# Performance work log

Measured on AMD Instinct MI355X. Metric: run time of the kernel, lower is better.

The kernel has to match this reference:

```python
import jax, jax.numpy as jnp
import numpy as np

SRC_V, TRG_V = 36616, 23262
EMB, ENC_H, DEC_H = 300, 512, 1024
S, T, B = 50, 50, 128


def setup_inputs() -> dict:
    key = jax.random.key(0)
    ks = jax.random.split(key, 17)
    sc = 0.05
    n = lambda k, shp: (jax.random.normal(k, shp, jnp.float32) * sc)
    return {
        "input_src_batch": jax.random.randint(ks[0], (S, B), 0, SRC_V),
        "input_trg_batch": jax.random.randint(ks[1], (T, B), 0, TRG_V),
        "EEMB": n(ks[2], (SRC_V, EMB)),
        "enc_Wih_f": n(ks[3], (4 * ENC_H, EMB)),
        "enc_Whh_f": n(ks[4], (4 * ENC_H, ENC_H)),
        "enc_b_f": n(ks[5], (4 * ENC_H,)),
        "enc_Wih_r": n(ks[6], (4 * ENC_H, EMB)),
        "enc_Whh_r": n(ks[7], (4 * ENC_H, ENC_H)),
        "enc_b_r": n(ks[8], (4 * ENC_H,)),
        "attn_Wi": n(ks[9], (DEC_H, DEC_H)),
        "attn_Wo": n(ks[10], (DEC_H, 2 * DEC_H)),
        "dec_Wih": n(ks[11], (4 * DEC_H, DEC_H + EMB)),
        "dec_Whh": n(ks[12], (4 * DEC_H, DEC_H)),
        "dec_b": n(ks[13], (4 * DEC_H,)),
        "DEMB": n(ks[14], (TRG_V, EMB)),
        "gen_W": n(ks[15], (TRG_V, DEC_H)),
        "gen_b": n(ks[16], (TRG_V,)),
    }


def lstm_step(h, c, x, Wih, Whh, b):
    # PyTorch gate order: i, f, g, o
    g = x @ Wih.T + h @ Whh.T + b
    i, f, gg, o = jnp.split(g, 4, axis=-1)
    c2 = jax.nn.sigmoid(f) * c + jax.nn.sigmoid(i) * jnp.tanh(gg)
    h2 = jax.nn.sigmoid(o) * jnp.tanh(c2)
    return h2, c2


def reference(input_src_batch, input_trg_batch, EEMB, enc_Wih_f, enc_Whh_f,
              enc_b_f, enc_Wih_r, enc_Whh_r, enc_b_r, attn_Wi, attn_Wo,
              dec_Wih, dec_Whh, dec_b, DEMB, gen_W, gen_b):
    batch = input_src_batch.shape[1]
    sent_len = input_trg_batch.shape[0]
    emb = EEMB[input_src_batch]  # [S, B, 300]

    def scan_dir(xs, Wih, Whh, b):
        def f(carry, x):
            h, c = carry
            h2, c2 = lstm_step(h, c, x, Wih, Whh, b)
            return (h2, c2), h2
        init = (jnp.zeros((batch, ENC_H), emb.dtype),
                jnp.zeros((batch, ENC_H), emb.dtype))
        (hF, cF), hs = jax.lax.scan(f, init, xs)
        return hs, hF, cF

    hs_f, hF, cF = scan_dir(emb, enc_Wih_f, enc_Whh_f, enc_b_f)
    hs_r, hR, cR = scan_dir(emb[::-1], enc_Wih_r, enc_Whh_r, enc_b_r)
    hs_r = hs_r[::-1]
    enc_out = jnp.concatenate([hs_f, hs_r], axis=-1)  # [S, B, 1024]
    # torch permute(1,2,0).view(B,1024) interleaves fwd/rev per feature
    hidden = jnp.stack([hF, hR], axis=-1).reshape(batch, DEC_H)
    context = jnp.stack([cF, cR], axis=-1).reshape(batch, DEC_H)

    def attn(h):
        semi = h @ attn_Wi.T                                # [B,1024]
        score = jnp.einsum('sbd,bd->sb', enc_out, semi)     # [S,B]
        alpha = jax.nn.softmax(score, axis=0)               # softmax over src len
        s_tilde = jnp.einsum('sb,sbd->bd', alpha, enc_out)  # [B,1024]
        return jnp.tanh(jnp.concatenate([s_tilde, h], axis=1) @ attn_Wo.T)

    trg_emb = DEMB[input_trg_batch[: sent_len - 1]]  # [T-1, B, 300]

    def step(carry, x_emb):
        h, c = carry
        c_t = attn(h)
        dec_in = jnp.concatenate([c_t, x_emb], axis=1)  # [B, 1324]
        h2, c2 = lstm_step(h, c, dec_in, dec_Wih, dec_Whh, dec_b)
        logp = jax.nn.log_softmax(h2 @ gen_W.T + gen_b, axis=1)
        return (h2, c2), logp

    _, outs = jax.lax.scan(step, (hidden, context), trg_emb)  # [T-1,B,V]
    out0 = jnp.zeros((1, batch, TRG_V), outs.dtype)
    return jnp.concatenate([out0, outs], axis=0)  # [T, B, V]
```

## Files before the change

kernel.cpp:

```cpp
#include <hip/hip_runtime.h>
#include <hip/hip_bf16.h>

#define S_LEN 50
#define T_LEN 50
#define BATCH 128
#define EMB 300
#define ENC_H 512
#define DEC_H 1024
#define TRG_V 23262
#define DEC_IN (DEC_H + EMB)
#define KCAT (DEC_IN + DEC_H)
#define GN (4 * DEC_H)

static inline int cdiv(int a, int b) { return (a + b - 1) / b; }

__device__ __forceinline__ float sigm(float x) { return 1.f / (1.f + expf(-x)); }

typedef __attribute__((ext_vector_type(8))) short bf16x8;
typedef __attribute__((ext_vector_type(4))) float f32x4;

__device__ __forceinline__ void gload_lds16(const void* g, void* l) {
    __builtin_amdgcn_global_load_lds((const __attribute__((address_space(1))) int*)g,
                                     (__attribute__((address_space(3))) int*)l, 16, 0, 0);
}

__device__ __forceinline__ float cload1(const float* p) {
    return __hip_atomic_load(p, __ATOMIC_RELAXED, __HIP_MEMORY_SCOPE_AGENT);
}
__device__ __forceinline__ float2 cload2(const float* p) {
    unsigned long long u = __hip_atomic_load((const unsigned long long*)p,
                                             __ATOMIC_RELAXED, __HIP_MEMORY_SCOPE_AGENT);
    union U { unsigned long long u; float2 f; } c; c.u = u; return c.f;
}
__device__ __forceinline__ float4 cload4(const float* p) {
    float2 a = cload2(p), b = cload2(p + 2);
    return make_float4(a.x, a.y, b.x, b.y);
}
__device__ __forceinline__ void cstore1(float* p, float v) {
    __hip_atomic_store(p, v, __ATOMIC_RELAXED, __HIP_MEMORY_SCOPE_AGENT);
}
__device__ __forceinline__ void cstore2(float* p, float2 v) {
    union U { unsigned long long u; float2 f; } c; c.f = v;
    __hip_atomic_store((unsigned long long*)p, c.u, __ATOMIC_RELAXED, __HIP_MEMORY_SCOPE_AGENT);
}
__device__ __forceinline__ void cstore4(float* p, float4 v) {
    cstore2(p, make_float2(v.x, v.y)); cstore2(p + 2, make_float2(v.z, v.w));
}

__device__ __forceinline__ void gbar(unsigned* cnt, unsigned target) {
    __syncthreads();
    if (threadIdx.x == 0) {
        atomicAdd(cnt, 1u);
        while (atomicAdd(cnt, 0u) < target)
            __builtin_amdgcn_s_sleep(32);
    }
    __syncthreads();
}

__global__ __launch_bounds__(256)
void gemm_mfma_bf16(const __hip_bfloat16* __restrict__ A, const __hip_bfloat16* __restrict__ W,
                    const float* __restrict__ bias, float* __restrict__ C,
                    int M, int N, int K, int ldc)
{
    __shared__ short As[128 * 32];
    __shared__ short Bs[128 * 32];
    const int tid  = threadIdx.x;
    const int wave = tid >> 6;
    const int lane = tid & 63;
    const int m0 = blockIdx.y * 128;
    const int n0 = blockIdx.x * 128;
    const int wr = wave >> 1, wc = wave & 1;

    const int srow = lane >> 2;
    const int kgrp = lane & 3;
    const int arow0 = 32 * wave;

    f32x4 acc[4][4] = {};

    for (int k0 = 0; k0 < K; k0 += 32) {
#pragma unroll
        for (int c = 0; c < 2; c++) {
            int row = arow0 + 16 * c + srow;
            gload_lds16(A + (size_t)(m0 + row) * K + k0 + kgrp * 8,
                        &As[(arow0 + 16 * c) * 32]);
        }
#pragma unroll
        for (int c = 0; c < 2; c++) {
            int row = arow0 + 16 * c + srow;
            int gr = n0 + row; if (gr > N - 1) gr = N - 1;
            gload_lds16(W + (size_t)gr * K + k0 + kgrp * 8,
                        &Bs[(arow0 + 16 * c) * 32]);
        }
        __syncthreads();

        bf16x8 a[4], b[4];
#pragma unroll
        for (int mi = 0; mi < 4; mi++)
            a[mi] = *(const bf16x8*)&As[(wr * 64 + mi * 16 + (lane & 15)) * 32 + (lane >> 4) * 8];
#pragma unroll
        for (int ni = 0; ni < 4; ni++)
            b[ni] = *(const bf16x8*)&Bs[(wc * 64 + ni * 16 + (lane & 15)) * 32 + (lane >> 4) * 8];
#pragma unroll
        for (int mi = 0; mi < 4; mi++)
#pragma unroll
            for (int ni = 0; ni < 4; ni++)
                acc[mi][ni] = __builtin_amdgcn_mfma_f32_16x16x32_bf16(a[mi], b[ni], acc[mi][ni], 0, 0, 0);
        __syncthreads();
    }

#pragma unroll
    for (int mi = 0; mi < 4; mi++)
#pragma unroll
        for (int ni = 0; ni < 4; ni++) {
            int col = n0 + wc * 64 + ni * 16 + (lane & 15);
            if (col >= N) continue;
            float bv = bias[col];
#pragma unroll
            for (int r = 0; r < 4; r++) {
                int row = m0 + wr * 64 + mi * 16 + (lane >> 4) * 4 + r;
                C[(size_t)row * ldc + col] = acc[mi][ni][r] + bv;
            }
        }
}

__global__ void cast_f32_bf16(const float* __restrict__ in, __hip_bfloat16* __restrict__ out, size_t n)
{
    size_t i = ((size_t)blockIdx.x * blockDim.x + threadIdx.x) * 4;
    if (i + 3 < n) {
        float4 v = *(const float4*)(in + i);
        out[i + 0] = __float2bfloat16(v.x);
        out[i + 1] = __float2bfloat16(v.y);
        out[i + 2] = __float2bfloat16(v.z);
        out[i + 3] = __float2bfloat16(v.w);
    } else {
        for (; i < n; i++) out[i] = __float2bfloat16(in[i]);
    }
}

template<int BM, int BN, int BK, int TM, int TN, bool HAS_BIAS>
__global__ __launch_bounds__((BM / TM) * (BN / TN))
void gemm_bt(const float* __restrict__ A, const float* __restrict__ W,
             const float* __restrict__ bias, float* __restrict__ C,
             int M, int N, int K, int ldc)
{
    constexpr int NT  = (BM / TM) * (BN / TN);
    constexpr int NGA = TM / 4;
    constexpr int NGB = TN / 4;
    constexpr int GS  = (BN / TN) * 4;
    constexpr int LPA = BM * BK / 4 / NT;
    constexpr int LPB = BN * BK / 4 / NT;

    __shared__ float As[BK][BM + 4];
    __shared__ float Bs[BK][BN + 4];

    const int tid = threadIdx.x;
    const int tx = tid % (BN / TN);
    const int ty = tid / (BN / TN);
    const int m0 = blockIdx.y * BM;
    const int n0 = blockIdx.x * BN;

    float acc[TM][TN];
#pragma unroll
    for (int i = 0; i < TM; i++)
#pragma unroll
        for (int j = 0; j < TN; j++) acc[i][j] = 0.f;

    for (int k0 = 0; k0 < K; k0 += BK) {
#pragma unroll
        for (int e = 0; e < LPA; e++) {
            int idx = tid + e * NT;
            int r = idx / (BK / 4);
            int c4 = idx % (BK / 4);
            int row = m0 + r; if (row > M - 1) row = M - 1;
            int kk = k0 + c4 * 4;
            float4 v;
            if (kk + 3 < K) {
                v = *(const float4*)(A + (size_t)row * K + kk);
            } else {
                v.x = (kk + 0 < K) ? A[(size_t)row * K + kk + 0] : 0.f;
                v.y = (kk + 1 < K) ? A[(size_t)row * K + kk + 1] : 0.f;
                v.z = (kk + 2 < K) ? A[(size_t)row * K + kk + 2] : 0.f;
                v.w = (kk + 3 < K) ? A[(size_t)row * K + kk + 3] : 0.f;
            }
            As[c4 * 4 + 0][r] = v.x; As[c4 * 4 + 1][r] = v.y;
            As[c4 * 4 + 2][r] = v.z; As[c4 * 4 + 3][r] = v.w;
        }
#pragma unroll
        for (int e = 0; e < LPB; e++) {
            int idx = tid + e * NT;
            int r = idx / (BK / 4);
            int c4 = idx % (BK / 4);
            int row = n0 + r; if (row > N - 1) row = N - 1;
            int kk = k0 + c4 * 4;
            float4 v;
            if (kk + 3 < K) {
                v = *(const float4*)(W + (size_t)row * K + kk);
            } else {
                v.x = (kk + 0 < K) ? W[(size_t)row * K + kk + 0] : 0.f;
                v.y = (kk + 1 < K) ? W[(size_t)row * K + kk + 1] : 0.f;
                v.z = (kk + 2 < K) ? W[(size_t)row * K + kk + 2] : 0.f;
                v.w = (kk + 3 < K) ? W[(size_t)row * K + kk + 3] : 0.f;
            }
            Bs[c4 * 4 + 0][r] = v.x; Bs[c4 * 4 + 1][r] = v.y;
            Bs[c4 * 4 + 2][r] = v.z; Bs[c4 * 4 + 3][r] = v.w;
        }
        __syncthreads();
#pragma unroll
        for (int kk = 0; kk < BK; kk++) {
            float a[TM], b[TN];
#pragma unroll
            for (int g = 0; g < NGA; g++) {
                float4 v = *(const float4*)(&As[kk][ty * TM + g * 4]);
                a[g * 4 + 0] = v.x; a[g * 4 + 1] = v.y; a[g * 4 + 2] = v.z; a[g * 4 + 3] = v.w;
            }
#pragma unroll
            for (int g = 0; g < NGB; g++) {
                float4 v = *(const float4*)(&Bs[kk][tx * 4 + g * GS]);
                b[g * 4 + 0] = v.x; b[g * 4 + 1] = v.y; b[g * 4 + 2] = v.z; b[g * 4 + 3] = v.w;
            }
#pragma unroll
            for (int i = 0; i < TM; i++)
#pragma unroll
                for (int j = 0; j < TN; j++)
                    acc[i][j] = fmaf(a[i], b[j], acc[i][j]);
        }
        __syncthreads();
    }

#pragma unroll
    for (int i = 0; i < TM; i++) {
        int row = m0 + ty * TM + i;
        if (row >= M) continue;
#pragma unroll
        for (int g = 0; g < NGB; g++) {
            int colb = n0 + tx * 4 + g * GS;
#pragma unroll
            for (int j = 0; j < 4; j++) {
                int cc = colb + j;
                if (cc >= N) continue;
                float v = acc[i][g * 4 + j];
                if (HAS_BIAS) v += bias[cc];
                C[(size_t)row * ldc + cc] = v;
            }
        }
    }
}

__device__ __forceinline__ float4 g4k(const float* base, int kk, int K) {
    float4 v = make_float4(0.f, 0.f, 0.f, 0.f);
    if (kk + 3 < K) v = *(const float4*)(base + kk);
    else {
        if (kk     < K) v.x = base[kk];
        if (kk + 1 < K) v.y = base[kk + 1];
        if (kk + 2 < K) v.z = base[kk + 2];
    }
    return v;
}
__device__ __forceinline__ float4 g4kc(const float* base, int kk, int K) {
    float4 v = make_float4(0.f, 0.f, 0.f, 0.f);
    if (kk + 3 < K) v = cload4(base + kk);
    else {
        if (kk     < K) v.x = cload1(base + kk);
        if (kk + 1 < K) v.y = cload1(base + kk + 1);
        if (kk + 2 < K) v.z = cload1(base + kk + 2);
    }
    return v;
}

__device__ __forceinline__ void tile_core(
    float (&As)[2][32][36], float (&Bs)[2][32][68],
    const float* __restrict__ A, int lda,
    const float* __restrict__ W, int ldw, int K,
    int m0, int n0, float (&acc)[2][4])
{
    const int tid = threadIdx.x;
    const int tx = tid & 15, ty = tid >> 4;
    const int ar = tid >> 3, ac4 = tid & 7;
    const float* abase = A + (size_t)(m0 + ar) * lda;
    const float* bb0   = W + (size_t)(n0 + ar) * ldw;
    const float* bb1   = bb0 + (size_t)32 * ldw;

    acc[0][0]=acc[0][1]=acc[0][2]=acc[0][3]=0.f;
    acc[1][0]=acc[1][1]=acc[1][2]=acc[1][3]=0.f;
    const int NIT = (K + 31) / 32;

    float4 pa0, pb00, pb10;
    float4 pa1, pb01, pb11;

    auto LOAD = [&](int itx, float4& qa, float4& qb0, float4& qb1) {
        int k0 = itx * 32, kk = k0 + ac4 * 4;
        if (k0 + 32 <= K) {
            qa = cload4(abase + kk); qb0 = *(const float4*)(bb0 + kk); qb1 = *(const float4*)(bb1 + kk);
        } else {
            qa = g4kc(abase, kk, K); qb0 = g4k(bb0, kk, K); qb1 = g4k(bb1, kk, K);
        }
    };
    auto SLDS = [&](int nb, const float4& qa, const float4& qb0, const float4& qb1) {
        *(float4*)&As[nb][ar][ac4 * 4] = qa;
        Bs[nb][ac4*4+0][ar]    = qb0.x; Bs[nb][ac4*4+1][ar]    = qb0.y;
        Bs[nb][ac4*4+2][ar]    = qb0.z; Bs[nb][ac4*4+3][ar]    = qb0.w;
        Bs[nb][ac4*4+0][ar+32] = qb1.x; Bs[nb][ac4*4+1][ar+32] = qb1.y;
        Bs[nb][ac4*4+2][ar+32] = qb1.z; Bs[nb][ac4*4+3][ar+32] = qb1.w;
    };
    auto COMP = [&](int c) {
#pragma unroll
        for (int k4 = 0; k4 < 8; ++k4) {
            float4 a0 = *(const float4*)&As[c][ty*2+0][k4*4];
            float4 a1 = *(const float4*)&As[c][ty*2+1][k4*4];
            float4 b0 = *(const float4*)&Bs[c][k4*4+0][tx*4];
            float4 b1 = *(const float4*)&Bs[c][k4*4+1][tx*4];
            float4 b2 = *(const float4*)&Bs[c][k4*4+2][tx*4];
            float4 b3 = *(const float4*)&Bs[c][k4*4+3][tx*4];
            float av0[4] = {a0.x, a0.y, a0.z, a0.w};
            float av1[4] = {a1.x, a1.y, a1.z, a1.w};
            float4 bq[4] = {b0, b1, b2, b3};
#pragma unroll
            for (int q = 0; q < 4; q++) {
                acc[0][0] = fmaf(av0[q], bq[q].x, acc[0][0]);
                acc[0][1] = fmaf(av0[q], bq[q].y, acc[0][1]);
                acc[0][2] = fmaf(av0[q], bq[q].z, acc[0][2]);
                acc[0][3] = fmaf(av0[q], bq[q].w, acc[0][3]);
                acc[1][0] = fmaf(av1[q], bq[q].x, acc[1][0]);
                acc[1][1] = fmaf(av1[q], bq[q].y, acc[1][1]);
                acc[1][2] = fmaf(av1[q], bq[q].z, acc[1][2]);
                acc[1][3] = fmaf(av1[q], bq[q].w, acc[1][3]);
            }
        }
    };

    LOAD(0, pa0, pb00, pb10);
    if (NIT > 1) LOAD(1, pa1, pb01, pb11);
    SLDS(0, pa0, pb00, pb10);
    __syncthreads();

    int cur = 0;
    int it = 0;
    while (it < NIT) {
        if (it + 2 < NIT) LOAD(it + 2, pa0, pb00, pb10);
        COMP(cur);
        if (it + 1 < NIT) SLDS(cur ^ 1, pa1, pb01, pb11);
        __syncthreads();
        cur ^= 1; ++it;
        if (it >= NIT) break;
        if (it + 2 < NIT) LOAD(it + 2, pa1, pb01, pb11);
        COMP(cur);
        if (it + 1 < NIT) SLDS(cur ^ 1, pa0, pb00, pb10);
        __syncthreads();
        cur ^= 1; ++it;
    }
}

__device__ __forceinline__ void attn_body(
    int b, float* hv, float* sc,
    const float* __restrict__ encP, const float* __restrict__ enc_out,
    float* __restrict__ attn_cat)
{
    const int tid = threadIdx.x;
    for (int d = tid; d < DEC_H; d += 256) hv[d] = cload1(&attn_cat[(size_t)b * 2 * DEC_H + DEC_H + d]);
    __syncthreads();
    int wave = tid >> 6, lane = tid & 63;
    for (int s = wave; s < S_LEN; s += 4) {
        const float* e = encP + ((size_t)s * BATCH + b) * DEC_H;
        float p = 0.f;
        for (int d = lane; d < DEC_H; d += 64) p = fmaf(e[d], hv[d], p);
        for (int off = 32; off; off >>= 1) p += __shfl_down(p, off);
        if (lane == 0) sc[s] = p;
    }
    __syncthreads();
    if (tid < 64) {
        float x = (tid < S_LEN) ? sc[tid] : -1e30f;
        float m = x;
        for (int off = 32; off; off >>= 1) m = fmaxf(m, __shfl_xor(m, off));
        float ex = (tid < S_LEN) ? expf(x - m) : 0.f;
        float ssum = ex;
        for (int off = 32; off; off >>= 1) ssum += __shfl_xor(ssum, off);
        if (tid < S_LEN) sc[tid] = ex / ssum;
    }
    __syncthreads();
    for (int d = tid; d < DEC_H; d += 256) {
        float a = 0.f;
#pragma unroll 5
        for (int s = 0; s < S_LEN; s++)
            a = fmaf(sc[s], enc_out[((size_t)s * BATCH + b) * DEC_H + d], a);
        cstore1(&attn_cat[(size_t)b * 2 * DEC_H + d], a);
    }
}

__global__ __launch_bounds__(256)
void enc_persistent(const float* __restrict__ Gf, const float* __restrict__ Gr,
                    const float* __restrict__ whhF, const float* __restrict__ whhR,
                    float* __restrict__ hF2, float* __restrict__ hR2,
                    float* __restrict__ cF, float* __restrict__ cR,
                    float* __restrict__ enc_out, unsigned* __restrict__ barcnt)
{
    __shared__ struct { float As[2][32][36]; float Bs[2][32][68]; } sm;
    const int blk = blockIdx.x;
    const int tid = threadIdx.x;
    const int tx = tid & 15, ty = tid >> 4;
    const int dir = blk >> 7;
    const int id  = blk & 127;
    const int m0 = (id >> 5) * 32;
    const int n0 = (id & 31) * 64;
    const float* W  = dir ? whhR : whhF;
    float* cst      = dir ? cR : cF;
    float* hbase    = dir ? hR2 : hF2;
    const float* G  = dir ? Gr : Gf;
    const int HS = BATCH * ENC_H;
    unsigned epoch = 0;
    float acc[2][4];

    for (int t = 0; t < S_LEN; ++t) {
        const float* h_in = hbase + (size_t)(t & 1) * HS;
        float* h_out      = hbase + (size_t)((t + 1) & 1) * HS;
        int s_g = dir ? (S_LEN - 1 - t) : t;
        const float* D = G + (size_t)s_g * BATCH * 4 * ENC_H;

        tile_core(sm.As, sm.Bs, h_in, ENC_H, W, ENC_H, ENC_H, m0, n0, acc);

        int cb = n0 + tx * 4, j = cb >> 2;
#pragma unroll
        for (int i = 0; i < 2; i++) {
            int b = m0 + ty * 2 + i;
            float4 d4 = *(const float4*)(D + (size_t)b * 4 * ENC_H + cb);
            float gi = acc[i][0] + d4.x, gf = acc[i][1] + d4.y;
            float gg = acc[i][2] + d4.z, go = acc[i][3] + d4.w;
            float c2 = sigm(gf) * cst[b * ENC_H + j] + sigm(gi) * tanhf(gg);
            float h2 = sigm(go) * tanhf(c2);
            cst[b * ENC_H + j] = c2;
            cstore1(&h_out[b * ENC_H + j], h2);
            enc_out[((size_t)s_g * BATCH + b) * DEC_H + dir * ENC_H + j] = h2;
        }
        if (t < S_LEN - 1) gbar(barcnt, 256u * (++epoch));
    }
}

__global__ __launch_bounds__(256)
void dec_persistent(const float* __restrict__ encP, const float* __restrict__ enc_out,
                    const int* __restrict__ trg, const float* __restrict__ DEMB,
                    const float* __restrict__ aWo, const float* __restrict__ wcat,
                    const float* __restrict__ db_i,
                    float* __restrict__ attn_cat, float* __restrict__ catA,
                    float* __restrict__ cdec, float* __restrict__ gpart,
                    __hip_bfloat16* __restrict__ H_bf, unsigned* __restrict__ barcnt)
{
    __shared__ union {
        struct { float hv[DEC_H]; float sc[S_LEN]; } a;
        struct { float As[2][32][36]; float Bs[2][32][68]; } g;
    } sm;
    const int blk = blockIdx.x;
    const int tid = threadIdx.x;
    const int tx = tid & 15, ty = tid >> 4;
    unsigned epoch = 0;
    float acc[2][4];

    for (int t = 0; t < T_LEN - 1; ++t) {
        if (blk < 128) {
            attn_body(blk, sm.a.hv, sm.a.sc, encP, enc_out, attn_cat);
        } else if (blk < 192) {
            int id = blk - 128;
            int m0 = (id >> 4) * 32, n0 = (id & 15) * 64;
            tile_core(sm.g.As, sm.g.Bs, attn_cat + DEC_H, 2 * DEC_H,
                      aWo + DEC_H, 2 * DEC_H, DEC_H, m0, n0, acc);
            int cb = n0 + tx * 4;
#pragma unroll
            for (int i = 0; i < 2; i++) {
                int row = m0 + ty * 2 + i;
                cstore4(catA + (size_t)row * KCAT + cb,
                        make_float4(acc[i][0], acc[i][1], acc[i][2], acc[i][3]));
            }
        } else {
            int tau = blk - 192;
            int m0 = (tau >> 6) * 32, n0 = (tau & 63) * 64;
            tile_core(sm.g.As, sm.g.Bs, catA + DEC_H, KCAT,
                      wcat + DEC_H, KCAT, KCAT - DEC_H, m0, n0, acc);
            int cb = n0 + tx * 4;
#pragma unroll
            for (int i = 0; i < 2; i++) {
                int row = m0 + ty * 2 + i;
                cstore4(gpart + (size_t)row * GN + cb,
                        make_float4(acc[i][0], acc[i][1], acc[i][2], acc[i][3]));
            }
        }
        gbar(barcnt, 256u * (++epoch));

        if (blk < 64) {
            int m0 = (blk >> 4) * 32, n0 = (blk & 15) * 64;
            tile_core(sm.g.As, sm.g.Bs, attn_cat, 2 * DEC_H, aWo, 2 * DEC_H, DEC_H, m0, n0, acc);
            int cb = n0 + tx * 4;
#pragma unroll
            for (int i = 0; i < 2; i++) {
                int row = m0 + ty * 2 + i;
                float* dst = catA + (size_t)row * KCAT + cb;
                float4 prev = cload4(dst);
                cstore4(dst, make_float4(tanhf(acc[i][0] + prev.x), tanhf(acc[i][1] + prev.y),
                                         tanhf(acc[i][2] + prev.z), tanhf(acc[i][3] + prev.w)));
            }
        } else {
            int tau = blk;
            int m0 = (tau >> 6) * 32, n0 = (tau & 63) * 64;
            tile_core(sm.g.As, sm.g.Bs, catA + DEC_H, KCAT,
                      wcat + DEC_H, KCAT, KCAT - DEC_H, m0, n0, acc);
            int cb = n0 + tx * 4;
#pragma unroll
            for (int i = 0; i < 2; i++) {
                int row = m0 + ty * 2 + i;
                cstore4(gpart + (size_t)row * GN + cb,
                        make_float4(acc[i][0], acc[i][1], acc[i][2], acc[i][3]));
            }
        }
        gbar(barcnt, 256u * (++epoch));

        {
            int m0 = (blk >> 6) * 32, n0 = (blk & 63) * 64;
            tile_core(sm.g.As, sm.g.Bs, catA, KCAT, wcat, KCAT, DEC_H, m0, n0, acc);
            int cb = n0 + tx * 4, j = cb >> 2;
            float4 bz = *(const float4*)(db_i + cb);
#pragma unroll
            for (int i = 0; i < 2; i++) {
                int b = m0 + ty * 2 + i;
                float4 gp = cload4(gpart + (size_t)b * GN + cb);
                float gi = acc[i][0] + gp.x + bz.x, gf = acc[i][1] + gp.y + bz.y;
                float gg = acc[i][2] + gp.z + bz.z, go = acc[i][3] + gp.w + bz.w;
                float c2 = sigm(gf) * cdec[b * DEC_H + j] + sigm(gi) * tanhf(gg);
                float h2 = sigm(go) * tanhf(c2);
                cdec[b * DEC_H + j] = c2;
                H_bf[(size_t)t * BATCH * DEC_H + b * DEC_H + j] = __float2bfloat16(h2);
                cstore1(&attn_cat[(size_t)b * 2 * DEC_H + DEC_H + j], h2);
                cstore1(&catA[(size_t)b * KCAT + DEC_IN + j], h2);
            }
            if ((blk & 63) == 0 && t + 1 < T_LEN - 1) {
                for (int idx = tid; idx < 32 * EMB; idx += 256) {
                    int r = m0 + idx / EMB, e = idx % EMB;
                    int idt = trg[(t + 1) * BATCH + r];
                    cstore1(&catA[(size_t)r * KCAT + DEC_H + e], DEMB[(size_t)idt * EMB + e]);
                }
            }
        }
        if (t < T_LEN - 2) gbar(barcnt, 256u * (++epoch));
    }
}

__global__ void zero_f32(float* p, size_t n) {
    size_t i = (size_t)blockIdx.x * blockDim.x + threadIdx.x;
    if (i < n) p[i] = 0.f;
}

__global__ void gather_rows(const int* __restrict__ ids, const float* __restrict__ E,
                            float* __restrict__ out, int nrows, int width)
{
    size_t i = (size_t)blockIdx.x * blockDim.x + threadIdx.x;
    size_t total = (size_t)nrows * width;
    if (i >= total) return;
    int r = (int)(i / width);
    int e = (int)(i % width);
    out[i] = E[(size_t)ids[r] * width + e];
}

__global__ void interleave_rows(const float* __restrict__ src, float* __restrict__ dst,
                                int units, int kdim)
{
    size_t i = (size_t)blockIdx.x * blockDim.x + threadIdx.x;
    size_t total = (size_t)4 * units * kdim;
    if (i >= total) return;
    int ir = (int)(i / kdim), k = (int)(i % kdim);
    int gate = ir & 3, j = ir >> 2;
    dst[i] = src[(size_t)(gate * units + j) * kdim + k];
}

__global__ void interleave_vec(const float* __restrict__ src, float* __restrict__ dst, int units)
{
    int i = blockIdx.x * blockDim.x + threadIdx.x;
    if (i >= 4 * units) return;
    int gate = i & 3, j = i >> 2;
    dst[i] = src[gate * units + j];
}

__global__ void build_wcat_int(const float* __restrict__ Wih, const float* __restrict__ Whh,
                               float* __restrict__ dst)
{
    size_t i = (size_t)blockIdx.x * blockDim.x + threadIdx.x;
    if (i >= (size_t)4 * DEC_H * KCAT) return;
    int ir = (int)(i / KCAT), k = (int)(i % KCAT);
    int gate = ir & 3, j = ir >> 2;
    int r = gate * DEC_H + j;
    dst[i] = (k < DEC_IN) ? Wih[(size_t)r * DEC_IN + k] : Whh[(size_t)r * DEC_H + (k - DEC_IN)];
}

__global__ void transpose_sq(const float* __restrict__ src, float* __restrict__ dst, int n)
{
    int i = blockIdx.x * blockDim.x + threadIdx.x;
    if (i >= n * n) return;
    int r = i / n, c = i % n;
    dst[(size_t)r * n + c] = src[(size_t)c * n + r];
}

__global__ void dec_init2(const float* __restrict__ hF, const float* __restrict__ cF,
                          const float* __restrict__ hR, const float* __restrict__ cR,
                          const int* __restrict__ trg, const float* __restrict__ DEMB,
                          float* __restrict__ attn_cat, float* __restrict__ catA,
                          float* __restrict__ cdec)
{
    int idx = blockIdx.x * blockDim.x + threadIdx.x;
    if (idx < BATCH * DEC_H) {
        int b = idx / DEC_H, j = idx % DEC_H;
        int half = j >> 1;
        float h = (j & 1) ? hR[b * ENC_H + half] : hF[b * ENC_H + half];
        float c = (j & 1) ? cR[b * ENC_H + half] : cF[b * ENC_H + half];
        attn_cat[(size_t)b * 2 * DEC_H + DEC_H + j] = h;
        catA[(size_t)b * KCAT + DEC_IN + j] = h;
        cdec[idx] = c;
    } else {
        int i = idx - BATCH * DEC_H;
        if (i >= BATCH * EMB) return;
        int b = i / EMB, e = i % EMB;
        catA[(size_t)b * KCAT + DEC_H + e] = DEMB[(size_t)trg[b] * EMB + e];
    }
}

__global__ __launch_bounds__(256)
void log_softmax_rows(float* __restrict__ X, int V)
{
    int row = blockIdx.x;
    float* x = X + (size_t)row * V;
    int tid = threadIdx.x;
    __shared__ float redm[4], reds[4];
    float m = -1e30f;
    for (int i = tid; i < V; i += 256) m = fmaxf(m, x[i]);
    for (int off = 32; off; off >>= 1) m = fmaxf(m, __shfl_xor(m, off));
    if ((tid & 63) == 0) redm[tid >> 6] = m;
    __syncthreads();
    m = fmaxf(fmaxf(redm[0], redm[1]), fmaxf(redm[2], redm[3]));
    float s = 0.f;
    for (int i = tid; i < V; i += 256) s += expf(x[i] - m);
    for (int off = 32; off; off >>= 1) s += __shfl_xor(s, off);
    if ((tid & 63) == 0) reds[tid >> 6] = s;
    __syncthreads();
    s = reds[0] + reds[1] + reds[2] + reds[3];
    float lg = m + logf(s);
    for (int i = tid; i < V; i += 256) x[i] -= lg;
}

static void launch_gemm_big_bias(const float* A, const float* W, const float* bias, float* C,
                                 int M, int N, int K, int ldc, hipStream_t s)
{
    dim3 g(cdiv(N, 128), cdiv(M, 128), 1);
    gemm_bt<128, 128, 16, 8, 8, true><<<g, 256, 0, s>>>(A, W, bias, C, M, N, K, ldc);
}
static void launch_gemm_big(const float* A, const float* W, float* C,
                            int M, int N, int K, int ldc, hipStream_t s)
{
    dim3 g(cdiv(N, 128), cdiv(M, 128), 1);
    gemm_bt<128, 128, 16, 8, 8, false><<<g, 256, 0, s>>>(A, W, nullptr, C, M, N, K, ldc);
}

extern "C" void kernel_launch(void* const* d_in, const int* in_sizes, int n_in,
                              void* d_out, int out_size, void* d_ws, size_t ws_size,
                              hipStream_t stream)
{
    const int*   src   = (const int*)d_in[0];
    const int*   trg   = (const int*)d_in[1];
    const float* EEMBp = (const float*)d_in[2];
    const float* eWihF = (const float*)d_in[3];
    const float* eWhhF = (const float*)d_in[4];
    const float* ebF   = (const float*)d_in[5];
    const float* eWihR = (const float*)d_in[6];
    const float* eWhhR = (const float*)d_in[7];
    const float* ebR   = (const float*)d_in[8];
    const float* aWi   = (const float*)d_in[9];
    const float* aWo   = (const float*)d_in[10];
    const float* dWih  = (const float*)d_in[11];
    const float* dWhh  = (const float*)d_in[12];
    const float* db    = (const float*)d_in[13];
    const float* DEMBp = (const float*)d_in[14];
    const float* gW    = (const float*)d_in[15];
    const float* gb    = (const float*)d_in[16];
    float* out = (float*)d_out;
    float* ws  = (float*)d_ws;

    size_t off = 0;
    auto alloc = [&](size_t n) { float* p = ws + off; off += n; return p; };

    float* Gf      = alloc((size_t)S_LEN * BATCH * 4 * ENC_H);
    float* Gr      = alloc((size_t)S_LEN * BATCH * 4 * ENC_H);
    float* emb_src = alloc((size_t)S_LEN * BATCH * EMB);
    float* enc_out = alloc((size_t)S_LEN * BATCH * DEC_H);
    float* hF2     = alloc((size_t)2 * BATCH * ENC_H);
    float* hR2     = alloc((size_t)2 * BATCH * ENC_H);
    float* cF      = alloc(BATCH * ENC_H);
    float* cR      = alloc(BATCH * ENC_H);
    float* wihF_i  = alloc((size_t)4 * ENC_H * EMB);
    float* wihR_i  = alloc((size_t)4 * ENC_H * EMB);
    float* whhF_i  = alloc((size_t)4 * ENC_H * ENC_H);
    float* whhR_i  = alloc((size_t)4 * ENC_H * ENC_H);
    float* ebF_i   = alloc(4 * ENC_H);
    float* ebR_i   = alloc(4 * ENC_H);
    float* wcat_i  = alloc((size_t)4 * DEC_H * KCAT);
    float* db_i    = alloc(4 * DEC_H);
    float* aWiT    = alloc((size_t)DEC_H * DEC_H);
    float* cdec    = alloc(BATCH * DEC_H);
    float* attn_cat= alloc((size_t)BATCH * 2 * DEC_H);
    float* catA    = alloc((size_t)BATCH * KCAT);
    float* gpart   = alloc((size_t)BATCH * GN);
    __hip_bfloat16* H_bf = (__hip_bfloat16*)alloc((size_t)(T_LEN - 1) * BATCH * DEC_H / 2);
    unsigned* barcnt = (unsigned*)alloc(16);
    __hip_bfloat16* gWb = (__hip_bfloat16*)Gf;
    float* encP = Gr;

    const int HS = BATCH * ENC_H;

    zero_f32<<<cdiv(BATCH * TRG_V, 256), 256, 0, stream>>>(out, (size_t)BATCH * TRG_V);
    zero_f32<<<cdiv(6 * HS, 256), 256, 0, stream>>>(hF2, (size_t)6 * HS);
    zero_f32<<<1, 16, 0, stream>>>((float*)barcnt, 16);

    gather_rows<<<cdiv(S_LEN * BATCH * EMB, 256), 256, 0, stream>>>(src, EEMBp, emb_src, S_LEN * BATCH, EMB);

    interleave_rows<<<cdiv(4 * ENC_H * EMB, 256), 256, 0, stream>>>(eWihF, wihF_i, ENC_H, EMB);
    interleave_rows<<<cdiv(4 * ENC_H * EMB, 256), 256, 0, stream>>>(eWihR, wihR_i, ENC_H, EMB);
    interleave_rows<<<cdiv(4 * ENC_H * ENC_H, 256), 256, 0, stream>>>(eWhhF, whhF_i, ENC_H, ENC_H);
    interleave_rows<<<cdiv(4 * ENC_H * ENC_H, 256), 256, 0, stream>>>(eWhhR, whhR_i, ENC_H, ENC_H);
    interleave_vec<<<cdiv(4 * ENC_H, 256), 256, 0, stream>>>(ebF, ebF_i, ENC_H);
    interleave_vec<<<cdiv(4 * ENC_H, 256), 256, 0, stream>>>(ebR, ebR_i, ENC_H);
    build_wcat_int<<<cdiv(4 * DEC_H * KCAT, 256), 256, 0, stream>>>(dWih, dWhh, wcat_i);
    interleave_vec<<<cdiv(4 * DEC_H, 256), 256, 0, stream>>>(db, db_i, DEC_H);
    transpose_sq<<<cdiv(DEC_H * DEC_H, 256), 256, 0, stream>>>(aWi, aWiT, DEC_H);

    launch_gemm_big_bias(emb_src, wihF_i, ebF_i, Gf, S_LEN * BATCH, 4 * ENC_H, EMB, 4 * ENC_H, stream);
    launch_gemm_big_bias(emb_src, wihR_i, ebR_i, Gr, S_LEN * BATCH, 4 * ENC_H, EMB, 4 * ENC_H, stream);

    enc_persistent<<<256, 256, 0, stream>>>(Gf, Gr, whhF_i, whhR_i, hF2, hR2, cF, cR,
                                            enc_out, &barcnt[0]);

    launch_gemm_big(enc_out, aWiT, encP, S_LEN * BATCH, DEC_H, DEC_H, DEC_H, stream);

    cast_f32_bf16<<<cdiv((int)((size_t)TRG_V * DEC_H / 4), 256), 256, 0, stream>>>(gW, gWb, (size_t)TRG_V * DEC_H);

    dec_init2<<<cdiv(BATCH * DEC_H + BATCH * EMB, 256), 256, 0, stream>>>(
        hF2, cF, hR2, cR, trg, DEMBp, attn_cat, catA, cdec);

    dec_persistent<<<256, 256, 0, stream>>>(encP, enc_out, trg, DEMBp, aWo, wcat_i, db_i,
                                            attn_cat, catA, cdec, gpart, H_bf, &barcnt[1]);

    {
        dim3 g(cdiv(TRG_V, 128), cdiv((T_LEN - 1) * BATCH, 128), 1);
        gemm_mfma_bf16<<<g, 256, 0, stream>>>(H_bf, gWb, gb, out + (size_t)BATCH * TRG_V,
                                              (T_LEN - 1) * BATCH, TRG_V, DEC_H, TRG_V);
    }

    log_softmax_rows<<<(T_LEN - 1) * BATCH, 256, 0, stream>>>(out + (size_t)BATCH * TRG_V, TRG_V);
}
```

Baseline: 12.52 ms.

## Store decoder weights and encoder outputs in fp16 for the persistent decoder

Converts the decoder LSTM concatenated weights, the attention output weights, and the projected and raw encoder outputs to fp16 before the persistent decoder kernel. The decoder reads these as half and widens to float, roughly halving the memory traffic of each recurrent step. The tile_core double-buffered prefetch is simplified from a two-stage register prefetch to a single-stage one. This adds cast kernels and lowers precision on the recurrent path, which could affect accuracy over 49 steps.

```diff
diff --git a/kernel.cpp b/kernel.cpp
--- a/kernel.cpp
+++ b/kernel.cpp
@@ -1,5 +1,6 @@
 #include <hip/hip_runtime.h>
 #include <hip/hip_bf16.h>
+#include <hip/hip_fp16.h>
 
 #define S_LEN 50
 #define T_LEN 50
@@ -15,6 +16,12 @@
 static inline int cdiv(int a, int b) { return (a + b - 1) / b; }
 
 __device__ __forceinline__ float sigm(float x) { return 1.f / (1.f + expf(-x)); }
+__device__ __forceinline__ float b2f(unsigned short u) {
+    union { float f; unsigned u; } c; c.u = ((unsigned)u) << 16; return c.f;
+}
+__device__ __forceinline__ float h2f(unsigned short u) {
+    __half_raw r; r.x = u; return __half2float(*(const __half*)&r);
+}
 
 typedef __attribute__((ext_vector_type(8))) short bf16x8;
 typedef __attribute__((ext_vector_type(4))) float f32x4;
@@ -137,9 +144,23 @@
     }
 }
 
+__global__ void cast_f32_fp16(const float* __restrict__ in, __half* __restrict__ out, size_t n)
+{
+    size_t i = ((size_t)blockIdx.x * blockDim.x + threadIdx.x) * 4;
+    if (i + 3 < n) {
+        float4 v = *(const float4*)(in + i);
+        out[i + 0] = __float2half(v.x);
+        out[i + 1] = __float2half(v.y);
+        out[i + 2] = __float2half(v.z);
+        out[i + 3] = __float2half(v.w);
+    } else {
+        for (; i < n; i++) out[i] = __float2half(in[i]);
+    }
+}
+
 template<int BM, int BN, int BK, int TM, int TN, bool HAS_BIAS>
 __global__ __launch_bounds__((BM / TM) * (BN / TN))
-void gemm_bt(const float* __restrict__ A, const float* __restrict__ W,
+void gemm_bt(const float* __restrict__ A, const float* __restrict__ W, int ldw,
              const float* __restrict__ bias, float* __restrict__ C,
              int M, int N, int K, int ldc)
 {
@@ -194,12 +215,12 @@
             int kk = k0 + c4 * 4;
             float4 v;
             if (kk + 3 < K) {
-                v = *(const float4*)(W + (size_t)row * K + kk);
+                v = *(const float4*)(W + (size_t)row * ldw + kk);
             } else {
-                v.x = (kk + 0 < K) ? W[(size_t)row * K + kk + 0] : 0.f;
-                v.y = (kk + 1 < K) ? W[(size_t)row * K + kk + 1] : 0.f;
-                v.z = (kk + 2 < K) ? W[(size_t)row * K + kk + 2] : 0.f;
-                v.w = (kk + 3 < K) ? W[(size_t)row * K + kk + 3] : 0.f;
+                v.x = (kk + 0 < K) ? W[(size_t)row * ldw + kk + 0] : 0.f;
+                v.y = (kk + 1 < K) ? W[(size_t)row * ldw + kk + 1] : 0.f;
+                v.z = (kk + 2 < K) ? W[(size_t)row * ldw + kk + 2] : 0.f;
+                v.w = (kk + 3 < K) ? W[(size_t)row * ldw + kk + 3] : 0.f;
             }
             Bs[c4 * 4 + 0][r] = v.x; Bs[c4 * 4 + 1][r] = v.y;
             Bs[c4 * 4 + 2][r] = v.z; Bs[c4 * 4 + 3][r] = v.w;
@@ -246,13 +267,22 @@
     }
 }
 
-__device__ __forceinline__ float4 g4k(const float* base, int kk, int K) {
+__device__ __forceinline__ float4 load4B(const float* p) { return *(const float4*)p; }
+__device__ __forceinline__ float4 load4B(const __half* p) {
+    ushort4 v = *(const ushort4*)p;
+    return make_float4(h2f(v.x), h2f(v.y), h2f(v.z), h2f(v.w));
+}
+__device__ __forceinline__ float ld1B(const float* p) { return *p; }
+__device__ __forceinline__ float ld1B(const __half* p) { return h2f(*(const unsigned short*)p); }
+
+template<typename TB>
+__device__ __forceinline__ float4 g4kB(const TB* base, int kk, int K) {
     float4 v = make_float4(0.f, 0.f, 0.f, 0.f);
-    if (kk + 3 < K) v = *(const float4*)(base + kk);
+    if (kk + 3 < K) v = load4B(base + kk);
     else {
-        if (kk     < K) v.x = base[kk];
-        if (kk + 1 < K) v.y = base[kk + 1];
-        if (kk + 2 < K) v.z = base[kk + 2];
+        if (kk     < K) v.x = ld1B(base + kk);
+        if (kk + 1 < K) v.y = ld1B(base + kk + 1);
+        if (kk + 2 < K) v.z = ld1B(base + kk + 2);
     }
     return v;
 }
@@ -267,50 +297,56 @@
     return v;
 }
 
+template<typename TB>
 __device__ __forceinline__ void tile_core(
     float (&As)[2][32][36], float (&Bs)[2][32][68],
     const float* __restrict__ A, int lda,
-    const float* __restrict__ W, int ldw, int K,
+    const TB* __restrict__ W, int ldw, int K,
     int m0, int n0, float (&acc)[2][4])
 {
     const int tid = threadIdx.x;
     const int tx = tid & 15, ty = tid >> 4;
     const int ar = tid >> 3, ac4 = tid & 7;
     const float* abase = A + (size_t)(m0 + ar) * lda;
-    const float* bb0   = W + (size_t)(n0 + ar) * ldw;
-    const float* bb1   = bb0 + (size_t)32 * ldw;
+    const TB* bb0      = W + (size_t)(n0 + ar) * ldw;
+    const TB* bb1      = bb0 + (size_t)32 * ldw;
 
     acc[0][0]=acc[0][1]=acc[0][2]=acc[0][3]=0.f;
     acc[1][0]=acc[1][1]=acc[1][2]=acc[1][3]=0.f;
     const int NIT = (K + 31) / 32;
 
-    float4 pa0, pb00, pb10;
-    float4 pa1, pb01, pb11;
-
-    auto LOAD = [&](int itx, float4& qa, float4& qb0, float4& qb1) {
-        int k0 = itx * 32, kk = k0 + ac4 * 4;
-        if (k0 + 32 <= K) {
-            qa = cload4(abase + kk); qb0 = *(const float4*)(bb0 + kk); qb1 = *(const float4*)(bb1 + kk);
-        } else {
-            qa = g4kc(abase, kk, K); qb0 = g4k(bb0, kk, K); qb1 = g4k(bb1, kk, K);
-        }
-    };
-    auto SLDS = [&](int nb, const float4& qa, const float4& qb0, const float4& qb1) {
-        *(float4*)&As[nb][ar][ac4 * 4] = qa;
-        Bs[nb][ac4*4+0][ar]    = qb0.x; Bs[nb][ac4*4+1][ar]    = qb0.y;
-        Bs[nb][ac4*4+2][ar]    = qb0.z; Bs[nb][ac4*4+3][ar]    = qb0.w;
-        Bs[nb][ac4*4+0][ar+32] = qb1.x; Bs[nb][ac4*4+1][ar+32] = qb1.y;
-        Bs[nb][ac4*4+2][ar+32] = qb1.z; Bs[nb][ac4*4+3][ar+32] = qb1.w;
-    };
-    auto COMP = [&](int c) {
+    float4 pa, pb0, pb1;
+    {
+        int kk = ac4 * 4;
+        pa  = cload4(abase + kk);
+        pb0 = load4B(bb0 + kk);
+        pb1 = load4B(bb1 + kk);
+    }
+    *(float4*)&As[0][ar][ac4 * 4] = pa;
+    Bs[0][ac4*4+0][ar]    = pb0.x; Bs[0][ac4*4+1][ar]    = pb0.y;
+    Bs[0][ac4*4+2][ar]    = pb0.z; Bs[0][ac4*4+3][ar]    = pb0.w;
+    Bs[0][ac4*4+0][ar+32] = pb1.x; Bs[0][ac4*4+1][ar+32] = pb1.y;
+    Bs[0][ac4*4+2][ar+32] = pb1.z; Bs[0][ac4*4+3][ar+32] = pb1.w;
+    __syncthreads();
+
+    int cur = 0;
+    for (int it = 0; it < NIT; ++it) {
+        float4 qa, qb0, qb1;
+        const bool has = (it + 1 < NIT);
+        if (has) {
+            int k0 = (it + 1) * 32;
+            int kk = k0 + ac4 * 4;
+            if (k0 + 32 <= K) { qa = cload4(abase + kk); qb0 = load4B(bb0 + kk); qb1 = load4B(bb1 + kk); }
+            else { qa = g4kc(abase, kk, K); qb0 = g4kB(bb0, kk, K); qb1 = g4kB(bb1, kk, K); }
+        }
 #pragma unroll
         for (int k4 = 0; k4 < 8; ++k4) {
-            float4 a0 = *(const float4*)&As[c][ty*2+0][k4*4];
-            float4 a1 = *(const float4*)&As[c][ty*2+1][k4*4];
-            float4 b0 = *(const float4*)&Bs[c][k4*4+0][tx*4];
-            float4 b1 = *(const float4*)&Bs[c][k4*4+1][tx*4];
-            float4 b2 = *(const float4*)&Bs[c][k4*4+2][tx*4];
-            float4 b3 = *(const float4*)&Bs[c][k4*4+3][tx*4];
+            float4 a0 = *(const float4*)&As[cur][ty*2+0][k4*4];
+            float4 a1 = *(const float4*)&As[cur][ty*2+1][k4*4];
+            float4 b0 = *(const float4*)&Bs[cur][k4*4+0][tx*4];
+            float4 b1 = *(const float4*)&Bs[cur][k4*4+1][tx*4];
+            float4 b2 = *(const float4*)&Bs[cur][k4*4+2][tx*4];
+            float4 b3 = *(const float4*)&Bs[cur][k4*4+3][tx*4];
             float av0[4] = {a0.x, a0.y, a0.z, a0.w};
             float av1[4] = {a1.x, a1.y, a1.z, a1.w};
             float4 bq[4] = {b0, b1, b2, b3};
@@ -326,33 +362,22 @@
                 acc[1][3] = fmaf(av1[q], bq[q].w, acc[1][3]);
             }
         }
-    };
-
-    LOAD(0, pa0, pb00, pb10);
-    if (NIT > 1) LOAD(1, pa1, pb01, pb11);
-    SLDS(0, pa0, pb00, pb10);
-    __syncthreads();
-
-    int cur = 0;
-    int it = 0;
-    while (it < NIT) {
-        if (it + 2 < NIT) LOAD(it + 2, pa0, pb00, pb10);
-        COMP(cur);
-        if (it + 1 < NIT) SLDS(cur ^ 1, pa1, pb01, pb11);
+        if (has) {
+            int nb = cur ^ 1;
+            *(float4*)&As[nb][ar][ac4 * 4] = qa;
+            Bs[nb][ac4*4+0][ar]    = qb0.x; Bs[nb][ac4*4+1][ar]    = qb0.y;
+            Bs[nb][ac4*4+2][ar]    = qb0.z; Bs[nb][ac4*4+3][ar]    = qb0.w;
+            Bs[nb][ac4*4+0][ar+32] = qb1.x; Bs[nb][ac4*4+1][ar+32] = qb1.y;
+            Bs[nb][ac4*4+2][ar+32] = qb1.z; Bs[nb][ac4*4+3][ar+32] = qb1.w;
+        }
         __syncthreads();
-        cur ^= 1; ++it;
-        if (it >= NIT) break;
-        if (it + 2 < NIT) LOAD(it + 2, pa1, pb01, pb11);
-        COMP(cur);
-        if (it + 1 < NIT) SLDS(cur ^ 1, pa0, pb00, pb10);
-        __syncthreads();
-        cur ^= 1; ++it;
+        cur ^= 1;
     }
 }
 
 __device__ __forceinline__ void attn_body(
     int b, float* hv, float* sc,
-    const float* __restrict__ encP, const float* __restrict__ enc_out,
+    const __half* __restrict__ encP, const __half* __restrict__ enc_out,
     float* __restrict__ attn_cat)
 {
     const int tid = threadIdx.x;
@@ -360,9 +385,9 @@
     __syncthreads();
     int wave = tid >> 6, lane = tid & 63;
     for (int s = wave; s < S_LEN; s += 4) {
-        const float* e = encP + ((size_t)s * BATCH + b) * DEC_H;
+        const unsigned short* e = (const unsigned short*)(encP + ((size_t)s * BATCH + b) * DEC_H);
         float p = 0.f;
-        for (int d = lane; d < DEC_H; d += 64) p = fmaf(e[d], hv[d], p);
+        for (int d = lane; d < DEC_H; d += 64) p = fmaf(h2f(e[d]), hv[d], p);
         for (int off = 32; off; off >>= 1) p += __shfl_down(p, off);
         if (lane == 0) sc[s] = p;
     }
@@ -379,9 +404,10 @@
     __syncthreads();
     for (int d = tid; d < DEC_H; d += 256) {
         float a = 0.f;
+        const unsigned short* eo = (const unsigned short*)enc_out;
 #pragma unroll 5
         for (int s = 0; s < S_LEN; s++)
-            a = fmaf(sc[s], enc_out[((size_t)s * BATCH + b) * DEC_H + d], a);
+            a = fmaf(sc[s], h2f(eo[((size_t)s * BATCH + b) * DEC_H + d]), a);
         cstore1(&attn_cat[(size_t)b * 2 * DEC_H + d], a);
     }
 }
@@ -415,7 +441,7 @@
         int s_g = dir ? (S_LEN - 1 - t) : t;
         const float* D = G + (size_t)s_g * BATCH * 4 * ENC_H;
 
-        tile_core(sm.As, sm.Bs, h_in, ENC_H, W, ENC_H, ENC_H, m0, n0, acc);
+        tile_core<float>(sm.As, sm.Bs, h_in, ENC_H, W, ENC_H, ENC_H, m0, n0, acc);
 
         int cb = n0 + tx * 4, j = cb >> 2;
 #pragma unroll
@@ -435,9 +461,9 @@
 }
 
 __global__ __launch_bounds__(256)
-void dec_persistent(const float* __restrict__ encP, const float* __restrict__ enc_out,
+void dec_persistent(const __half* __restrict__ encP, const __half* __restrict__ enc_out,
                     const int* __restrict__ trg, const float* __restrict__ DEMB,
-                    const float* __restrict__ aWo, const float* __restrict__ wcat,
+                    const __half* __restrict__ aWo, const __half* __restrict__ wcat,
                     const float* __restrict__ db_i,
                     float* __restrict__ attn_cat, float* __restrict__ catA,
                     float* __restrict__ cdec, float* __restrict__ gpart,
@@ -459,8 +485,8 @@
         } else if (blk < 192) {
             int id = blk - 128;
             int m0 = (id >> 4) * 32, n0 = (id & 15) * 64;
-            tile_core(sm.g.As, sm.g.Bs, attn_cat + DEC_H, 2 * DEC_H,
-                      aWo + DEC_H, 2 * DEC_H, DEC_H, m0, n0, acc);
+            tile_core<__half>(sm.g.As, sm.g.Bs, attn_cat + DEC_H, 2 * DEC_H,
+                              aWo + DEC_H, 2 * DEC_H, DEC_H, m0, n0, acc);
             int cb = n0 + tx * 4;
 #pragma unroll
             for (int i = 0; i < 2; i++) {
@@ -471,8 +497,8 @@
         } else {
             int tau = blk - 192;
             int m0 = (tau >> 6) * 32, n0 = (tau & 63) * 64;
-            tile_core(sm.g.As, sm.g.Bs, catA + DEC_H, KCAT,
-                      wcat + DEC_H, KCAT, KCAT - DEC_H, m0, n0, acc);
+            tile_core<__half>(sm.g.As, sm.g.Bs, catA + DEC_H, KCAT,
+                              wcat + DEC_H, KCAT, KCAT - DEC_H, m0, n0, acc);
             int cb = n0 + tx * 4;
 #pragma unroll
             for (int i = 0; i < 2; i++) {
@@ -485,7 +511,8 @@
 
         if (blk < 64) {
             int m0 = (blk >> 4) * 32, n0 = (blk & 15) * 64;
-            tile_core(sm.g.As, sm.g.Bs, attn_cat, 2 * DEC_H, aWo, 2 * DEC_H, DEC_H, m0, n0, acc);
+            tile_core<__half>(sm.g.As, sm.g.Bs, attn_cat, 2 * DEC_H,
+                              aWo, 2 * DEC_H, DEC_H, m0, n0, acc);
             int cb = n0 + tx * 4;
 #pragma unroll
             for (int i = 0; i < 2; i++) {
@@ -498,8 +525,8 @@
         } else {
             int tau = blk;
             int m0 = (tau >> 6) * 32, n0 = (tau & 63) * 64;
-            tile_core(sm.g.As, sm.g.Bs, catA + DEC_H, KCAT,
-                      wcat + DEC_H, KCAT, KCAT - DEC_H, m0, n0, acc);
+            tile_core<__half>(sm.g.As, sm.g.Bs, catA + DEC_H, KCAT,
+                              wcat + DEC_H, KCAT, KCAT - DEC_H, m0, n0, acc);
             int cb = n0 + tx * 4;
 #pragma unroll
             for (int i = 0; i < 2; i++) {
@@ -512,7 +539,7 @@
 
         {
             int m0 = (blk >> 6) * 32, n0 = (blk & 63) * 64;
-            tile_core(sm.g.As, sm.g.Bs, catA, KCAT, wcat, KCAT, DEC_H, m0, n0, acc);
+            tile_core<__half>(sm.g.As, sm.g.Bs, catA, KCAT, wcat, KCAT, DEC_H, m0, n0, acc);
             int cb = n0 + tx * 4, j = cb >> 2;
             float4 bz = *(const float4*)(db_i + cb);
 #pragma unroll
@@ -575,15 +602,16 @@
     dst[i] = src[gate * units + j];
 }
 
-__global__ void build_wcat_int(const float* __restrict__ Wih, const float* __restrict__ Whh,
-                               float* __restrict__ dst)
+__global__ void build_wcat_fp16(const float* __restrict__ Wih, const float* __restrict__ Whh,
+                                __half* __restrict__ dst)
 {
     size_t i = (size_t)blockIdx.x * blockDim.x + threadIdx.x;
-    if (i >= (size_t)4 * DEC_H * KCAT) return;
+    if (i >= (size_t)GN * KCAT) return;
     int ir = (int)(i / KCAT), k = (int)(i % KCAT);
     int gate = ir & 3, j = ir >> 2;
     int r = gate * DEC_H + j;
-    dst[i] = (k < DEC_IN) ? Wih[(size_t)r * DEC_IN + k] : Whh[(size_t)r * DEC_H + (k - DEC_IN)];
+    float v = (k < DEC_IN) ? Wih[(size_t)r * DEC_IN + k] : Whh[(size_t)r * DEC_H + (k - DEC_IN)];
+    dst[i] = __float2half(v);
 }
 
 __global__ void transpose_sq(const float* __restrict__ src, float* __restrict__ dst, int n)
@@ -640,17 +668,17 @@
     for (int i = tid; i < V; i += 256) x[i] -= lg;
 }
 
-static void launch_gemm_big_bias(const float* A, const float* W, const float* bias, float* C,
-                                 int M, int N, int K, int ldc, hipStream_t s)
+static void launch_gemm_big_bias(const float* A, const float* W, int ldw, const float* bias,
+                                 float* C, int M, int N, int K, int ldc, hipStream_t s)
 {
     dim3 g(cdiv(N, 128), cdiv(M, 128), 1);
-    gemm_bt<128, 128, 16, 8, 8, true><<<g, 256, 0, s>>>(A, W, bias, C, M, N, K, ldc);
-}
-static void launch_gemm_big(const float* A, const float* W, float* C,
+    gemm_bt<128, 128, 16, 8, 8, true><<<g, 256, 0, s>>>(A, W, ldw, bias, C, M, N, K, ldc);
+}
+static void launch_gemm_big(const float* A, const float* W, int ldw, float* C,
                             int M, int N, int K, int ldc, hipStream_t s)
 {
     dim3 g(cdiv(N, 128), cdiv(M, 128), 1);
-    gemm_bt<128, 128, 16, 8, 8, false><<<g, 256, 0, s>>>(A, W, nullptr, C, M, N, K, ldc);
+    gemm_bt<128, 128, 16, 8, 8, false><<<g, 256, 0, s>>>(A, W, ldw, nullptr, C, M, N, K, ldc);
 }
 
 extern "C" void kernel_launch(void* const* d_in, const int* in_sizes, int n_in,
@@ -694,13 +722,16 @@
     float* whhR_i  = alloc((size_t)4 * ENC_H * ENC_H);
     float* ebF_i   = alloc(4 * ENC_H);
     float* ebR_i   = alloc(4 * ENC_H);
-    float* wcat_i  = alloc((size_t)4 * DEC_H * KCAT);
     float* db_i    = alloc(4 * DEC_H);
     float* aWiT    = alloc((size_t)DEC_H * DEC_H);
     float* cdec    = alloc(BATCH * DEC_H);
     float* attn_cat= alloc((size_t)BATCH * 2 * DEC_H);
     float* catA    = alloc((size_t)BATCH * KCAT);
     float* gpart   = alloc((size_t)BATCH * GN);
+    __half* wcat_hf = (__half*)alloc((size_t)GN * KCAT / 2);
+    __half* aWo_hf  = (__half*)alloc((size_t)DEC_H * 2 * DEC_H / 2);
+    __half* encP_hf = (__half*)alloc((size_t)S_LEN * BATCH * DEC_H / 2);
+    __half* eout_hf = (__half*)alloc((size_t)S_LEN * BATCH * DEC_H / 2);
     __hip_bfloat16* H_bf = (__hip_bfloat16*)alloc((size_t)(T_LEN - 1) * BATCH * DEC_H / 2);
     unsigned* barcnt = (unsigned*)alloc(16);
     __hip_bfloat16* gWb = (__hip_bfloat16*)Gf;
@@ -720,24 +751,30 @@
     interleave_rows<<<cdiv(4 * ENC_H * ENC_H, 256), 256, 0, stream>>>(eWhhR, whhR_i, ENC_H, ENC_H);
     interleave_vec<<<cdiv(4 * ENC_H, 256), 256, 0, stream>>>(ebF, ebF_i, ENC_H);
     interleave_vec<<<cdiv(4 * ENC_H, 256), 256, 0, stream>>>(ebR, ebR_i, ENC_H);
-    build_wcat_int<<<cdiv(4 * DEC_H * KCAT, 256), 256, 0, stream>>>(dWih, dWhh, wcat_i);
+    build_wcat_fp16<<<cdiv(GN * KCAT, 256), 256, 0, stream>>>(dWih, dWhh, wcat_hf);
+    cast_f32_fp16<<<cdiv((int)((size_t)DEC_H * 2 * DEC_H / 4), 256), 256, 0, stream>>>(
+        aWo, aWo_hf, (size_t)DEC_H * 2 * DEC_H);
     interleave_vec<<<cdiv(4 * DEC_H, 256), 256, 0, stream>>>(db, db_i, DEC_H);
     transpose_sq<<<cdiv(DEC_H * DEC_H, 256), 256, 0, stream>>>(aWi, aWiT, DEC_H);
 
-    launch_gemm_big_bias(emb_src, wihF_i, ebF_i, Gf, S_LEN * BATCH, 4 * ENC_H, EMB, 4 * ENC_H, stream);
-    launch_gemm_big_bias(emb_src, wihR_i, ebR_i, Gr, S_LEN * BATCH, 4 * ENC_H, EMB, 4 * ENC_H, stream);
+    launch_gemm_big_bias(emb_src, wihF_i, EMB, ebF_i, Gf, S_LEN * BATCH, 4 * ENC_H, EMB, 4 * ENC_H, stream);
+    launch_gemm_big_bias(emb_src, wihR_i, EMB, ebR_i, Gr, S_LEN * BATCH, 4 * ENC_H, EMB, 4 * ENC_H, stream);
 
     enc_persistent<<<256, 256, 0, stream>>>(Gf, Gr, whhF_i, whhR_i, hF2, hR2, cF, cR,
                                             enc_out, &barcnt[0]);
 
-    launch_gemm_big(enc_out, aWiT, encP, S_LEN * BATCH, DEC_H, DEC_H, DEC_H, stream);
+    launch_gemm_big(enc_out, aWiT, DEC_H, encP, S_LEN * BATCH, DEC_H, DEC_H, DEC_H, stream);
+    cast_f32_fp16<<<cdiv((int)((size_t)S_LEN * BATCH * DEC_H / 4), 256), 256, 0, stream>>>(
+        encP, encP_hf, (size_t)S_LEN * BATCH * DEC_H);
+    cast_f32_fp16<<<cdiv((int)((size_t)S_LEN * BATCH * DEC_H / 4), 256), 256, 0, stream>>>(
+        enc_out, eout_hf, (size_t)S_LEN * BATCH * DEC_H);
 
     cast_f32_bf16<<<cdiv((int)((size_t)TRG_V * DEC_H / 4), 256), 256, 0, stream>>>(gW, gWb, (size_t)TRG_V * DEC_H);
 
     dec_init2<<<cdiv(BATCH * DEC_H + BATCH * EMB, 256), 256, 0, stream>>>(
         hF2, cF, hR2, cR, trg, DEMBp, attn_cat, catA, cdec);
 
-    dec_persistent<<<256, 256, 0, stream>>>(encP, enc_out, trg, DEMBp, aWo, wcat_i, db_i,
+    dec_persistent<<<256, 256, 0, stream>>>(encP_hf, eout_hf, trg, DEMBp, aWo_hf, wcat_hf, db_i,
                                             attn_cat, catA, cdec, gpart, H_bf, &barcnt[1]);
 
     {
```

After: 12.59 ms. About the same (+0.6%).
